# Kernel tuning notes

Measured on AMD Instinct MI355X. Metric: run time of the kernel, lower is better.

Reference implementation:

```python
import jax, jax.numpy as jnp
import numpy as np
from jax.scipy.special import logsumexp

G, E, K, D, B, L, M, KN = 32000, 256, 8, 6, 4, 512, 64, 4
STEP, EPS = 0.05, 1.0


def setup_inputs() -> dict:
    key = jax.random.key(0)
    ks = jax.random.split(key, 16)
    s = 0.05  # weight scale for numerical stability
    return {
        'masked': jax.random.randint(ks[0], (B, L), 0, G),
        'unmasked': jax.random.randint(ks[1], (B, L), 0, G),
        'mask': jax.random.randint(ks[2], (B, M), 0, L),
        'summer': jnp.ones((B, M), jnp.float32),
        'embed': jax.random.normal(ks[3], (G, E), jnp.float32) * s,
        'pos': jax.random.normal(ks[4], (L, E), jnp.float32) * s,
        'Wt': jax.random.normal(ks[5], (D, E, E), jnp.float32) * s,
        'Wc': jax.random.normal(ks[6], (D, E, E), jnp.float32) * s,
        'Wq': jax.random.normal(ks[7], (D, K * E, E), jnp.float32) * s,
        'Wd': jax.random.normal(ks[8], (D, K * E, K * E), jnp.float32) * s,
        'Wo': jax.random.normal(ks[9], (D, K * E, E), jnp.float32) * s,
        'Wkc': jax.random.normal(ks[10], (E * KN, E), jnp.float32) * s,
        'bkc': jax.random.normal(ks[11], (E * KN,), jnp.float32) * s,
        'Wem': jax.random.normal(ks[12], (E, E), jnp.float32) * s,
    }


def _norm(x):
    # y / (eps + y.std(-1, unbiased)); torch std is ddof=1
    return x / (EPS + jnp.std(x, axis=-1, ddof=1, keepdims=True))


def reference(masked, unmasked, mask, summer, embed, pos, Wt, Wc, Wq, Wd, Wo, Wkc, bkc, Wem):
    b, l = masked.shape
    # batch init: token + positional embedding, normalized
    xsa = _norm(embed[masked] + pos[None, :l])  # (B,L,E)
    inv_sqrt_e = 1.0 / (E ** 0.5)
    for d in range(D):
        # local transition terms (roll +/- 1 along sequence)
        xsad = jax.nn.relu(jnp.roll(xsa, 1, axis=1) @ Wt[d]) @ Wc[d]
        xsad = xsad + jax.nn.relu(jnp.roll(xsa, -1, axis=1) @ Wc[d].T) @ Wt[d].T
        # QKV_Attention: K query heads against raw xsa keys/values
        q = (xsa @ Wq[d].T).reshape(b, l, K, E)           # (B,L,K,E)
        hijk = jnp.einsum('blke,bme->blkm', q, xsa) * inv_sqrt_e  # (B,L,K,L)
        pijk = jax.nn.softmax(hijk, axis=-1)
        yik = jnp.einsum('blkm,bme->blke', pijk, xsa)      # (B,L,K,E)
        xid = yik.reshape(b, l, K * E)
        # Dense -> ReLU -> Dense (mode 1)
        xidact = jax.nn.relu(xid @ Wd[d].T)                # (B,L,K*E)
        xsad = xsad + xidact @ Wo[d]                       # (B,L,E)
        # gradnorm + residual update + layernorm
        xsad = _norm(xsad)
        xsa = _norm(xsa + STEP * xsad)
    # loss head: gather masked positions
    lptok = jnp.take_along_axis(xsa, mask[:, :, None], axis=1)  # (B,M,E)
    m = mask.shape[1]
    xx = (lptok @ Wkc.T + bkc).reshape(b, m * KN, E)       # kchoice
    xx = jnp.einsum('bne,ble->bnl', xx, xsa)               # (B,M*KN,L)
    xx = jnp.einsum('bnl,ble->bne', xx, xsa)               # (B,M*KN,E)
    logits = (xx @ Wem) @ embed.T                          # (B,M*KN,G)
    k_lp = jax.nn.log_softmax(logits, axis=-1).reshape(b, m, KN, G)
    lp = logsumexp(k_lp, axis=-2) - jnp.float32(np.log(KN))  # (B,M,G)
    tgt = jnp.take_along_axis(unmasked, mask, axis=1)       # (B,M)
    cent = jnp.take_along_axis(lp, tgt[:, :, None], axis=-1)[:, :, 0]
    loss = -(cent * summer).sum(-1) / jnp.clip(summer.sum(-1), 1.0, None)
    return loss
```

## Files before the change

kernel.cpp:

```cpp
#include <hip/hip_runtime.h>
#include <math.h>
#include <stdint.h>

#define G_ 32000
#define E_ 256
#define K_ 8
#define D_ 6
#define B_ 4
#define L_ 512
#define M_ 64
#define KN_ 4
#define STEP_ 0.05f
#define BL_ (B_ * L_)
#define KE_ (K_ * E_)
#define NSPLIT_ 50
#define GCH_ 10

typedef __attribute__((ext_vector_type(8))) short short8;
typedef __attribute__((ext_vector_type(4))) float f32x4;
typedef __attribute__((ext_vector_type(4))) short short4v;

__device__ __forceinline__ short f2bf(float f) {
  unsigned u = __builtin_bit_cast(unsigned, f);
  unsigned r = (u + 0x7fffu + ((u >> 16) & 1u)) >> 16;
  return (short)r;
}

__device__ __forceinline__ void gload16(const void* g, void* l) {
  __builtin_amdgcn_global_load_lds(
      reinterpret_cast<const __attribute__((address_space(1))) void*>(
          reinterpret_cast<uintptr_t>(g)),
      reinterpret_cast<__attribute__((address_space(3))) void*>(
          reinterpret_cast<uintptr_t>(l)),
      16, 0, 0);
}

__device__ __forceinline__ float wsum(float v) {
#pragma unroll
  for (int o = 32; o > 0; o >>= 1) v += __shfl_xor(v, o, 64);
  return v;
}
__device__ __forceinline__ float block_sum(float v, float* sm) {
  v = wsum(v);
  int wid = threadIdx.x >> 6, lane = threadIdx.x & 63;
  if (lane == 0) sm[wid] = v;
  __syncthreads();
  float r = sm[0] + sm[1] + sm[2] + sm[3];
  __syncthreads();
  return r;
}

template <bool RELU, bool OBF>
__global__ __launch_bounds__(256) void mg128x64_k(
    const short* __restrict__ A, const short* __restrict__ B,
    void* __restrict__ Cg, int Kd, int lda, int ldb, int ldc) {
  __shared__ short As[128 * 64];
  __shared__ short Bs[64 * 64];
  int m0 = blockIdx.y * 128, n0 = blockIdx.x * 64;
  int t = threadIdx.x, w = t >> 6, l = t & 63;
  int l16 = l & 15, qd = l >> 4, hi8 = qd * 8;
  int wr_ = w >> 1, wc_ = w & 1;
  int sr = l >> 3;
  int scol = ((l & 7) * 8) ^ (sr << 3);
  f32x4 acc[4][2];
#pragma unroll
  for (int i = 0; i < 4; i++)
#pragma unroll
    for (int j = 0; j < 2; j++) acc[i][j] = {0.f, 0.f, 0.f, 0.f};

  for (int k0 = 0; k0 < Kd; k0 += 64) {
    __syncthreads();
#pragma unroll
    for (int c = 0; c < 4; c++) {
      int sub = w * 4 + c;
      int r = sub * 8 + sr;
      gload16(A + (long)(m0 + r) * lda + k0 + scol, &As[sub * 512]);
    }
#pragma unroll
    for (int c = 0; c < 2; c++) {
      int sub = w * 2 + c;
      int r = sub * 8 + sr;
      gload16(B + (long)(n0 + r) * ldb + k0 + scol, &Bs[sub * 512]);
    }
    __syncthreads();
#pragma unroll
    for (int ks = 0; ks < 2; ks++) {
      short8 af[4], bf[2];
#pragma unroll
      for (int rf = 0; rf < 4; rf++) {
        int row = wr_ * 64 + rf * 16 + l16;
        af[rf] = *(const short8*)&As[(row * 64 + ks * 32 + hi8) ^ ((row & 7) << 3)];
      }
#pragma unroll
      for (int cf = 0; cf < 2; cf++) {
        int row = wc_ * 32 + cf * 16 + l16;
        bf[cf] = *(const short8*)&Bs[(row * 64 + ks * 32 + hi8) ^ ((row & 7) << 3)];
      }
#pragma unroll
      for (int rf = 0; rf < 4; rf++)
#pragma unroll
        for (int cf = 0; cf < 2; cf++)
          acc[rf][cf] = __builtin_amdgcn_mfma_f32_16x16x32_bf16(
              af[rf], bf[cf], acc[rf][cf], 0, 0, 0);
    }
  }
#pragma unroll
  for (int rf = 0; rf < 4; rf++) {
#pragma unroll
    for (int cf = 0; cf < 2; cf++) {
      int col = n0 + wc_ * 32 + cf * 16 + l16;
#pragma unroll
      for (int j = 0; j < 4; j++) {
        int row = m0 + wr_ * 64 + rf * 16 + qd * 4 + j;
        float v = acc[rf][cf][j];
        if (RELU) v = fmaxf(v, 0.f);
        long idx = (long)row * ldc + col;
        if (OBF) ((short*)Cg)[idx] = f2bf(v);
        else ((float*)Cg)[idx] = v;
      }
    }
  }
}

__global__ __launch_bounds__(256) void mg64sk_k(
    const short* __restrict__ A, const short* __restrict__ B,
    float* __restrict__ P, int Klen, int lda, int ldb, int ldc, long pstride) {
  __shared__ short As[64 * 64];
  __shared__ short Bs[64 * 64];
  int z = blockIdx.z;
  int kbase = z * Klen;
  int m0 = blockIdx.y * 64, n0 = blockIdx.x * 64;
  int t = threadIdx.x, w = t >> 6, l = t & 63;
  int l16 = l & 15, qd = l >> 4, hi8 = qd * 8;
  int wr_ = w >> 1, wc_ = w & 1;
  int sr = l >> 3;
  int scol = ((l & 7) * 8) ^ (sr << 3);
  f32x4 acc[2][2];
#pragma unroll
  for (int i = 0; i < 2; i++)
#pragma unroll
    for (int j = 0; j < 2; j++) acc[i][j] = {0.f, 0.f, 0.f, 0.f};

  for (int k0 = 0; k0 < Klen; k0 += 64) {
    __syncthreads();
#pragma unroll
    for (int c = 0; c < 2; c++) {
      int sub = w * 2 + c;
      int r = sub * 8 + sr;
      gload16(A + (long)(m0 + r) * lda + kbase + k0 + scol, &As[sub * 512]);
      gload16(B + (long)(n0 + r) * ldb + kbase + k0 + scol, &Bs[sub * 512]);
    }
    __syncthreads();
#pragma unroll
    for (int ks = 0; ks < 2; ks++) {
      short8 af[2], bf[2];
#pragma unroll
      for (int rf = 0; rf < 2; rf++) {
        int row = wr_ * 32 + rf * 16 + l16;
        af[rf] = *(const short8*)&As[(row * 64 + ks * 32 + hi8) ^ ((row & 7) << 3)];
      }
#pragma unroll
      for (int cf = 0; cf < 2; cf++) {
        int row = wc_ * 32 + cf * 16 + l16;
        bf[cf] = *(const short8*)&Bs[(row * 64 + ks * 32 + hi8) ^ ((row & 7) << 3)];
      }
#pragma unroll
      for (int rf = 0; rf < 2; rf++)
#pragma unroll
        for (int cf = 0; cf < 2; cf++)
          acc[rf][cf] = __builtin_amdgcn_mfma_f32_16x16x32_bf16(
              af[rf], bf[cf], acc[rf][cf], 0, 0, 0);
    }
  }
  float* Pz = P + z * pstride;
#pragma unroll
  for (int rf = 0; rf < 2; rf++) {
#pragma unroll
    for (int cf = 0; cf < 2; cf++) {
      int col = n0 + wc_ * 32 + cf * 16 + l16;
#pragma unroll
      for (int j = 0; j < 4; j++) {
        int row = m0 + wr_ * 32 + rf * 16 + qd * 4 + j;
        Pz[(long)row * ldc + col] = acc[rf][cf][j];
      }
    }
  }
}

__global__ __launch_bounds__(256) void tpair_k(
    const short* __restrict__ xsa_bf, const short* __restrict__ wtT,
    const short* __restrict__ wcb, short* __restrict__ T) {
  __shared__ short As[64 * 64];
  __shared__ short Bs[64 * 64];
  int z = blockIdx.z;
  const short* Bb = z ? wcb : wtT;
  int rollv = z ? -1 : 1;
  int m0 = blockIdx.y * 64, n0 = blockIdx.x * 64;
  int t = threadIdx.x, w = t >> 6, l = t & 63;
  int l16 = l & 15, qd = l >> 4, hi8 = qd * 8;
  int wr_ = w >> 1, wc_ = w & 1;
  int sr = l >> 3;
  int scol = ((l & 7) * 8) ^ (sr << 3);
  f32x4 acc[2][2];
#pragma unroll
  for (int i = 0; i < 2; i++)
#pragma unroll
    for (int j = 0; j < 2; j++) acc[i][j] = {0.f, 0.f, 0.f, 0.f};
  for (int k0 = 0; k0 < E_; k0 += 64) {
    __syncthreads();
#pragma unroll
    for (int c = 0; c < 2; c++) {
      int sub = w * 2 + c;
      int r = sub * 8 + sr;
      int gr = m0 + r;
      int bb = gr >> 9, pp = gr & (L_ - 1);
      gr = (bb << 9) | ((pp - rollv + L_) & (L_ - 1));
      gload16(xsa_bf + (long)gr * E_ + k0 + scol, &As[sub * 512]);
      gload16(Bb + (long)(n0 + sub * 8 + sr) * E_ + k0 + scol, &Bs[sub * 512]);
    }
    __syncthreads();
#pragma unroll
    for (int ks = 0; ks < 2; ks++) {
      short8 af[2], bf[2];
#pragma unroll
      for (int rf = 0; rf < 2; rf++) {
        int row = wr_ * 32 + rf * 16 + l16;
        af[rf] = *(const short8*)&As[(row * 64 + ks * 32 + hi8) ^ ((row & 7) << 3)];
      }
#pragma unroll
      for (int cf = 0; cf < 2; cf++) {
        int row = wc_ * 32 + cf * 16 + l16;
        bf[cf] = *(const short8*)&Bs[(row * 64 + ks * 32 + hi8) ^ ((row & 7) << 3)];
      }
#pragma unroll
      for (int rf = 0; rf < 2; rf++)
#pragma unroll
        for (int cf = 0; cf < 2; cf++)
          acc[rf][cf] = __builtin_amdgcn_mfma_f32_16x16x32_bf16(
              af[rf], bf[cf], acc[rf][cf], 0, 0, 0);
    }
  }
#pragma unroll
  for (int rf = 0; rf < 2; rf++) {
#pragma unroll
    for (int cf = 0; cf < 2; cf++) {
      int col = n0 + wc_ * 32 + cf * 16 + l16;
#pragma unroll
      for (int j = 0; j < 4; j++) {
        int row = m0 + wr_ * 32 + rf * 16 + qd * 4 + j;
        T[(long)row * 512 + z * 256 + col] = f2bf(fmaxf(acc[rf][cf][j], 0.f));
      }
    }
  }
}

__global__ __launch_bounds__(512, 2) void flash3_k(
    const short* __restrict__ q_bf, const short* __restrict__ xsa_bf,
    const short* __restrict__ xsaT_bf, short* __restrict__ y_bf) {
  __shared__ short smem[69888];
  float* Obuf = (float*)smem;
  float* mst = (float*)&smem[69632];
  float* lst = mst + 64;
  int q0 = blockIdx.x * 64, hk = blockIdx.y, b = blockIdx.z;
  int t = threadIdx.x, w = t >> 6, l = t & 63;
  int l16 = l & 15, qd = l >> 4, hi8 = qd * 8;
  int qb = w & 3, half = w >> 2;
  const float scale = 0.0625f;

  short8 qf[8];
  {
    const short* qrow =
        q_bf + (long)(b * L_ + q0 + qb * 16 + l16) * KE_ + hk * 256;
#pragma unroll
    for (int ks = 0; ks < 8; ks++)
      qf[ks] = *(const short8*)(qrow + ks * 32 + hi8);
  }
  f32x4 acc_o[16];
#pragma unroll
  for (int i = 0; i < 16; i++) acc_o[i] = {0.f, 0.f, 0.f, 0.f};
  float mreg[4], lreg[4];
#pragma unroll
  for (int j = 0; j < 4; j++) { mreg[j] = -1e30f; lreg[j] = 0.f; }

  auto STAGE = [&](int nbuf, int it) {
#pragma unroll
    for (int c = 0; c < 4; c++) {
      int ch = w * 4 + c, hh = ch >> 4, rp = ch & 15;
      int row = rp * 2 + (l >> 5);
      int colsw = ((l & 31) * 8) ^ ((row & 7) << 3);
      gload16(xsa_bf + (long)(b * L_ + hh * 256 + it * 32 + row) * E_ + colsw,
              &smem[(nbuf * 2 + hh) * 8192 + rp * 512]);
    }
#pragma unroll
    for (int c = 0; c < 4; c++) {
      int ch = w * 4 + c, hh = ch >> 4, rg = ch & 15;
      int er = rg * 16 + (l >> 2);
      int col = (l & 3) * 8;
      gload16(xsaT_bf + (long)(b * E_ + er) * L_ + hh * 256 + it * 32 + col,
              &smem[32768 + (nbuf * 2 + hh) * 8192 + rg * 512]);
    }
  };

  STAGE(0, 0);
  __syncthreads();
  int cur = 0;
  for (int it = 0; it < 8; it++) {
    if (it < 7) STAGE(cur ^ 1, it + 1);
    const short* Kb = &smem[(cur * 2 + half) * 8192];
    const short* Vb = &smem[32768 + (cur * 2 + half) * 8192];
    short* Pw = &smem[65536 + w * 512];
    f32x4 s4[2];
    s4[0] = {0.f, 0.f, 0.f, 0.f};
    s4[1] = {0.f, 0.f, 0.f, 0.f};
#pragma unroll
    for (int ks = 0; ks < 8; ks++) {
#pragma unroll
      for (int cf = 0; cf < 2; cf++) {
        int row = cf * 16 + l16;
        short8 kb = *(const short8*)&Kb[row * 256 +
                                        ((ks * 32 + hi8) ^ ((row & 7) << 3))];
        s4[cf] = __builtin_amdgcn_mfma_f32_16x16x32_bf16(qf[ks], kb, s4[cf], 0, 0, 0);
      }
    }
    float alpha[4];
#pragma unroll
    for (int j = 0; j < 4; j++) {
      float v0 = s4[0][j] * scale, v1 = s4[1][j] * scale;
      float rmax = fmaxf(v0, v1);
#pragma unroll
      for (int mk = 1; mk <= 8; mk <<= 1) rmax = fmaxf(rmax, __shfl_xor(rmax, mk, 64));
      float mn = fmaxf(mreg[j], rmax);
      float p0 = __expf(v0 - mn), p1 = __expf(v1 - mn);
      float ps = p0 + p1;
#pragma unroll
      for (int mk = 1; mk <= 8; mk <<= 1) ps += __shfl_xor(ps, mk, 64);
      alpha[j] = __expf(mreg[j] - mn);
      lreg[j] = lreg[j] * alpha[j] + ps;
      mreg[j] = mn;
      int r = qd * 4 + j;
      Pw[r * 32 + l16] = f2bf(p0);
      Pw[r * 32 + 16 + l16] = f2bf(p1);
    }
#pragma unroll
    for (int cfo = 0; cfo < 16; cfo++)
#pragma unroll
      for (int j = 0; j < 4; j++) acc_o[cfo][j] *= alpha[j];
    short8 pa = *(const short8*)&Pw[l16 * 32 + hi8];
#pragma unroll
    for (int cfo = 0; cfo < 16; cfo++) {
      int er = cfo * 16 + l16;
      short8 vb = *(const short8*)&Vb[er * 32 + hi8];
      acc_o[cfo] = __builtin_amdgcn_mfma_f32_16x16x32_bf16(pa, vb, acc_o[cfo], 0, 0, 0);
    }
    __syncthreads();
    cur ^= 1;
  }
  if (half == 1) {
#pragma unroll
    for (int cfo = 0; cfo < 16; cfo++)
#pragma unroll
      for (int j = 0; j < 4; j++)
        Obuf[qb * 4096 + (qd * 4 + j) * 256 + cfo * 16 + l16] = acc_o[cfo][j];
    if (l16 == 0) {
#pragma unroll
      for (int j = 0; j < 4; j++) {
        mst[qb * 16 + qd * 4 + j] = mreg[j];
        lst[qb * 16 + qd * 4 + j] = lreg[j];
      }
    }
  }
  __syncthreads();
  if (half == 0) {
#pragma unroll
    for (int j = 0; j < 4; j++) {
      int r = qd * 4 + j;
      float m1 = mst[qb * 16 + r], l1 = lst[qb * 16 + r];
      float mn = fmaxf(mreg[j], m1);
      float a0 = __expf(mreg[j] - mn), a1 = __expf(m1 - mn);
      float linv = 1.0f / (lreg[j] * a0 + l1 * a1);
      short* yrow = y_bf + (long)(b * L_ + q0 + qb * 16 + r) * KE_ + hk * 256;
#pragma unroll
      for (int cfo = 0; cfo < 16; cfo++) {
        float o1 = Obuf[qb * 4096 + r * 256 + cfo * 16 + l16];
        yrow[cfo * 16 + l16] = f2bf((acc_o[cfo][j] * a0 + o1 * a1) * linv);
      }
    }
  }
}

__global__ __launch_bounds__(256) void finish_k(
    const float* __restrict__ Ptr, const float* __restrict__ Pwo,
    float* __restrict__ xsa, short* __restrict__ xsa_bf,
    short* __restrict__ xsaT_bf) {
  long r = blockIdx.x;
  int b = (int)(r / L_), ll = (int)(r % L_);
  int t = threadIdx.x;
  __shared__ float sm[4];
  long off = r * E_ + t;
  const long ps = (long)BL_ * E_;
  float vd = Ptr[off] + Ptr[ps + off] + Pwo[off] + Pwo[ps + off] +
             Pwo[2 * ps + off] + Pwo[3 * ps + off];
  float s1 = block_sum(vd, sm);
  float s2 = block_sum(vd * vd, sm);
  float mean = s1 * (1.0f / E_);
  float var = (s2 - s1 * mean) * (1.0f / (E_ - 1));
  float vdn = vd / (1.0f + sqrtf(fmaxf(var, 0.f)));
  float u = xsa[off] + STEP_ * vdn;
  s1 = block_sum(u, sm);
  s2 = block_sum(u * u, sm);
  mean = s1 * (1.0f / E_);
  var = (s2 - s1 * mean) * (1.0f / (E_ - 1));
  float xn = u / (1.0f + sqrtf(fmaxf(var, 0.f)));
  xsa[off] = xn;
  short h = f2bf(xn);
  xsa_bf[off] = h;
  xsaT_bf[((long)b * E_ + t) * L_ + ll] = h;
}

__global__ __launch_bounds__(256) void lse2_k(
    const short* __restrict__ tmat_bf, const short* __restrict__ embed_bf,
    float* __restrict__ mpart, float* __restrict__ spart) {
  __shared__ short Bs[64 * 256];
  int split = blockIdx.x, rb = blockIdx.y;
  int t = threadIdx.x, w = t >> 6, l = t & 63;
  int l16 = l & 15, qd = l >> 4, hi8 = qd * 8;
  short8 areg[8];
  {
    const short* ar = tmat_bf + (long)(rb * 64 + w * 16 + l16) * E_;
#pragma unroll
    for (int ks = 0; ks < 8; ks++) areg[ks] = *(const short8*)(ar + ks * 32 + hi8);
  }
  float m[4], s[4];
#pragma unroll
  for (int j = 0; j < 4; j++) { m[j] = -1e30f; s[j] = 0.f; }
  long gbase = (long)split * (GCH_ * 64);
  for (int ch = 0; ch < GCH_; ch++) {
    long g0 = gbase + ch * 64;
    __syncthreads();
#pragma unroll
    for (int j = 0; j < 8; j++) {
      int sub = w * 8 + j;
      int r = sub * 2 + (l >> 5);
      int col = ((l & 31) * 8) ^ ((r & 7) << 3);
      gload16(embed_bf + (g0 + r) * E_ + col, &Bs[sub * 512]);
    }
    __syncthreads();
    f32x4 acc[4];
#pragma unroll
    for (int cf = 0; cf < 4; cf++) acc[cf] = {0.f, 0.f, 0.f, 0.f};
#pragma unroll
    for (int ks = 0; ks < 8; ks++) {
#pragma unroll
      for (int cf = 0; cf < 4; cf++) {
        int row = cf * 16 + l16;
        short8 b = *(const short8*)&Bs[(row * 256 + ks * 32 + hi8) ^ ((row & 7) << 3)];
        acc[cf] = __builtin_amdgcn_mfma_f32_16x16x32_bf16(areg[ks], b, acc[cf], 0, 0, 0);
      }
    }
#pragma unroll
    for (int j = 0; j < 4; j++) {
      float vm = fmaxf(fmaxf(acc[0][j], acc[1][j]), fmaxf(acc[2][j], acc[3][j]));
      float mn = fmaxf(m[j], vm);
      s[j] = s[j] * __expf(m[j] - mn) + __expf(acc[0][j] - mn) +
             __expf(acc[1][j] - mn) + __expf(acc[2][j] - mn) +
             __expf(acc[3][j] - mn);
      m[j] = mn;
    }
  }
#pragma unroll
  for (int j = 0; j < 4; j++) {
#pragma unroll
    for (int mask = 1; mask <= 8; mask <<= 1) {
      float mo = __shfl_xor(m[j], mask, 64);
      float so = __shfl_xor(s[j], mask, 64);
      float mn = fmaxf(m[j], mo);
      s[j] = s[j] * __expf(m[j] - mn) + so * __expf(mo - mn);
      m[j] = mn;
    }
    if (l16 == 0) {
      int row = rb * 64 + w * 16 + qd * 4 + j;
      mpart[(long)row * NSPLIT_ + split] = m[j];
      spart[(long)row * NSPLIT_ + split] = s[j];
    }
  }
}

__device__ __forceinline__ void cvt_blk(const float* __restrict__ src,
                                        short* __restrict__ dst, int blk, int t) {
  int i = blk * 256 + t;
  float4 v = ((const float4*)src)[i];
  short4v o = {f2bf(v.x), f2bf(v.y), f2bf(v.z), f2bf(v.w)};
  ((short4v*)dst)[i] = o;
}
__device__ __forceinline__ void trans_blk(const float* __restrict__ src,
                                          short* __restrict__ dst, int bx, int by,
                                          int C, int ldd, float (*tile)[33], int t) {
  int c0 = bx * 32, r0 = by * 32;
  int tx = t & 31, ty = t >> 5;
#pragma unroll
  for (int k = 0; k < 4; k++)
    tile[ty + k * 8][tx] = src[(long)(r0 + ty + k * 8) * C + c0 + tx];
  __syncthreads();
#pragma unroll
  for (int k = 0; k < 4; k++)
    dst[(long)(c0 + ty + k * 8) * ldd + r0 + tx] = f2bf(tile[tx][ty + k * 8]);
}
#define LBLK_ 5376
__global__ __launch_bounds__(256) void wcvt_all_k(
    const float* __restrict__ embed, const float* __restrict__ Wt,
    const float* __restrict__ Wc, const float* __restrict__ Wq,
    const float* __restrict__ Wd, const float* __restrict__ Wo,
    short* embed_bf, short* wcb, short* wq, short* wd, short* wtT, short* woT,
    short* wcat) {
  __shared__ float tile[32][33];
  int blk = blockIdx.x, t = threadIdx.x;
  if (blk < 8000) { cvt_blk(embed, embed_bf, blk, t); return; }
  blk -= 8000;
  int d = blk / LBLK_;
  blk -= d * LBLK_;
  const float* Wt_d = Wt + (long)d * E_ * E_;
  const float* Wc_d = Wc + (long)d * E_ * E_;
  const float* Wq_d = Wq + (long)d * KE_ * E_;
  const float* Wd_d = Wd + (long)d * KE_ * KE_;
  const float* Wo_d = Wo + (long)d * KE_ * E_;
  short* wcb_d = wcb + (long)d * E_ * E_;
  short* wq_d = wq + (long)d * KE_ * E_;
  short* wd_d = wd + (long)d * KE_ * KE_;
  short* wtT_d = wtT + (long)d * E_ * E_;
  short* woT_d = woT + (long)d * E_ * KE_;
  short* wcat_d = wcat + (long)d * E_ * 512;
  if (blk < 4096) { cvt_blk(Wd_d, wd_d, blk, t); return; }
  blk -= 4096;
  if (blk < 512) { cvt_blk(Wq_d, wq_d, blk, t); return; }
  blk -= 512;
  if (blk < 64) { cvt_blk(Wc_d, wcb_d, blk, t); return; }
  blk -= 64;
  if (blk < 64) { trans_blk(Wt_d, wtT_d, blk & 7, blk >> 3, E_, E_, tile, t); return; }
  blk -= 64;
  if (blk < 512) { trans_blk(Wo_d, woT_d, blk & 7, blk >> 3, E_, KE_, tile, t); return; }
  blk -= 512;
  if (blk < 64) { trans_blk(Wc_d, wcat_d, blk & 7, blk >> 3, E_, 512, tile, t); return; }
  blk -= 64;
  {
    int i = blk * 256 + t;
    int n = i >> 6, kc = (i & 63) * 4;
    float4 v = *(const float4*)(Wt_d + (long)n * E_ + kc);
    short4v o = {f2bf(v.x), f2bf(v.y), f2bf(v.z), f2bf(v.w)};
    *(short4v*)(wcat_d + (long)n * 512 + 256 + kc) = o;
  }
}

__global__ __launch_bounds__(256) void cvt_k(const float* __restrict__ src,
                                             short* __restrict__ dst, int n4) {
  int i = blockIdx.x * 256 + threadIdx.x;
  if (i < n4) {
    float4 v = ((const float4*)src)[i];
    short4v o = {f2bf(v.x), f2bf(v.y), f2bf(v.z), f2bf(v.w)};
    ((short4v*)dst)[i] = o;
  }
}

__global__ __launch_bounds__(256) void embed_init_k(
    const int* __restrict__ masked, const float* __restrict__ embed,
    const float* __restrict__ pos, float* __restrict__ xsa,
    short* __restrict__ xsa_bf, short* __restrict__ xsaT_bf) {
  int bl = blockIdx.x;
  int b = bl / L_, ll = bl % L_;
  int t = threadIdx.x;
  __shared__ float sm[4];
  int tok = masked[bl];
  float v = embed[(long)tok * E_ + t] + pos[(long)ll * E_ + t];
  float s1 = block_sum(v, sm);
  float s2 = block_sum(v * v, sm);
  float mean = s1 * (1.0f / E_);
  float var = (s2 - s1 * mean) * (1.0f / (E_ - 1));
  float xn = v / (1.0f + sqrtf(fmaxf(var, 0.f)));
  xsa[(long)bl * E_ + t] = xn;
  short h = f2bf(xn);
  xsa_bf[(long)bl * E_ + t] = h;
  xsaT_bf[((long)b * E_ + t) * L_ + ll] = h;
}

__global__ __launch_bounds__(256) void gather_k(const float* __restrict__ xsa,
                                                const int* __restrict__ mask,
                                                float* __restrict__ lptok) {
  int bm = blockIdx.x;
  int b = bm >> 6;
  int t = threadIdx.x;
  int p = mask[bm];
  lptok[(long)bm * E_ + t] = xsa[((long)b * L_ + p) * E_ + t];
}

template <bool TRB, bool BIAS>
__global__ __launch_bounds__(256) void gemm_k(
    const float* __restrict__ Ag, const float* __restrict__ Bg,
    float* __restrict__ Cg, const float* __restrict__ bias, int M, int N,
    int Kd, int lda, int ldb, int ldc, long sA1, long sB1, long sC1) {
  constexpr int BM = 64, BN = 64, BK = 16, TM = 4, TN = 4;
  int b1 = blockIdx.z;
  const float* A = Ag + b1 * sA1;
  const float* Bp = Bg + b1 * sB1;
  float* C = Cg + b1 * sC1;
  int m0 = blockIdx.y * BM, n0 = blockIdx.x * BN;
  __shared__ float As[BK][BM + 4];
  __shared__ float Bs[BK][BN + 4];
  int t = threadIdx.x;
  int tx = t % (BN / TN), ty = t / (BN / TN);
  float acc[TM][TN];
#pragma unroll
  for (int i = 0; i < TM; i++)
#pragma unroll
    for (int j = 0; j < TN; j++) acc[i][j] = 0.f;
  for (int k0 = 0; k0 < Kd; k0 += BK) {
    __syncthreads();
    {
      int r = t / (BK / 4), kc = (t % (BK / 4)) * 4;
      float4 v = *(const float4*)(A + (long)(m0 + r) * lda + k0 + kc);
      As[kc + 0][r] = v.x;
      As[kc + 1][r] = v.y;
      As[kc + 2][r] = v.z;
      As[kc + 3][r] = v.w;
    }
    if (!TRB) {
      int r = t / (BN / 4), nc = (t % (BN / 4)) * 4;
      *(float4*)(&Bs[r][nc]) = *(const float4*)(Bp + (long)(k0 + r) * ldb + n0 + nc);
    } else {
      int n = t / (BK / 4), kc = (t % (BK / 4)) * 4;
      float4 v = *(const float4*)(Bp + (long)(n0 + n) * ldb + k0 + kc);
      Bs[kc + 0][n] = v.x;
      Bs[kc + 1][n] = v.y;
      Bs[kc + 2][n] = v.z;
      Bs[kc + 3][n] = v.w;
    }
    __syncthreads();
#pragma unroll
    for (int kk = 0; kk < BK; kk++) {
      float a[TM], b[TN];
#pragma unroll
      for (int i = 0; i < TM; i++) a[i] = As[kk][ty * TM + i];
#pragma unroll
      for (int j = 0; j < TN; j++) b[j] = Bs[kk][tx * TN + j];
#pragma unroll
      for (int i = 0; i < TM; i++)
#pragma unroll
        for (int j = 0; j < TN; j++) acc[i][j] = fmaf(a[i], b[j], acc[i][j]);
    }
  }
#pragma unroll
  for (int i = 0; i < TM; i++) {
    long row = m0 + ty * TM + i;
    float* cp = C + row * (long)ldc + n0 + tx * TN;
#pragma unroll
    for (int j = 0; j < TN; j++) {
      float v = acc[i][j];
      if (BIAS) v += bias[n0 + tx * TN + j];
      cp[j] = v;
    }
  }
}

__global__ __launch_bounds__(256) void cent_k(
    const float* __restrict__ tmat, const float* __restrict__ embed,
    const int* __restrict__ mask, const int* __restrict__ unmasked,
    const float* __restrict__ mpart, const float* __restrict__ spart,
    float* __restrict__ cent) {
  int bm = blockIdx.x;
  int b = bm >> 6, m = bm & 63;
  int t = threadIdx.x;
  __shared__ float sm[4];
  __shared__ float tlv[KN_];
  int pos = mask[bm];
  int tgt = unmasked[b * L_ + pos];
  float ev = embed[(long)tgt * E_ + t];
  for (int kn = 0; kn < KN_; kn++) {
    long grow = (long)b * (M_ * KN_) + m * KN_ + kn;
    float dot = block_sum(tmat[grow * E_ + t] * ev, sm);
    if (t == 0) {
      float M = -1e30f, S = 0.f;
      for (int i = 0; i < NSPLIT_; i++) {
        float m2 = mpart[grow * NSPLIT_ + i], s2 = spart[grow * NSPLIT_ + i];
        float MM = fmaxf(M, m2);
        S = S * __expf(M - MM) + s2 * __expf(m2 - MM);
        M = MM;
      }
      tlv[kn] = dot - (M + __logf(S));
    }
  }
  __syncthreads();
  if (t == 0) {
    float mx = fmaxf(fmaxf(tlv[0], tlv[1]), fmaxf(tlv[2], tlv[3]));
    float s = __expf(tlv[0] - mx) + __expf(tlv[1] - mx) + __expf(tlv[2] - mx) +
              __expf(tlv[3] - mx);
    cent[bm] = __logf(s) + mx - 1.3862943611198906f;
  }
}

__global__ __launch_bounds__(256) void loss_k(const float* __restrict__ cent,
                                              const float* __restrict__ summer,
                                              float* __restrict__ out) {
  int t = threadIdx.x;
  int b = t >> 6, m = t & 63;
  float c = cent[b * 64 + m], su = summer[b * 64 + m];
  float num = wsum(c * su);
  float den = wsum(su);
  if (m == 0) out[b] = -num / fmaxf(den, 1.0f);
}

extern "C" void kernel_launch(void* const* d_in, const int* in_sizes, int n_in,
                              void* d_out, int out_size, void* d_ws,
                              size_t ws_size, hipStream_t stream) {
  (void)in_sizes; (void)n_in; (void)out_size; (void)ws_size;
  const int* masked = (const int*)d_in[0];
  const int* unmasked = (const int*)d_in[1];
  const int* mask = (const int*)d_in[2];
  const float* summer = (const float*)d_in[3];
  const float* embed = (const float*)d_in[4];
  const float* pos = (const float*)d_in[5];
  const float* Wt = (const float*)d_in[6];
  const float* Wc = (const float*)d_in[7];
  const float* Wq = (const float*)d_in[8];
  const float* Wd = (const float*)d_in[9];
  const float* Wo = (const float*)d_in[10];
  const float* Wkc = (const float*)d_in[11];
  const float* bkc = (const float*)d_in[12];
  const float* Wem = (const float*)d_in[13];
  float* out = (float*)d_out;

  char* p = (char*)d_ws;
  auto take = [&](size_t bytes) {
    char* r = p;
    p += (bytes + 255) & ~(size_t)255;
    return r;
  };
  float* xsa = (float*)take((size_t)BL_ * E_ * 4);
  short* xsa_bf = (short*)take((size_t)BL_ * E_ * 2);
  short* xsaT_bf = (short*)take((size_t)BL_ * E_ * 2);
  short* t_buf = (short*)take((size_t)BL_ * 512 * 2);
  short* q_bf = (short*)take((size_t)BL_ * KE_ * 2);
  short* y_bf = (short*)take((size_t)BL_ * KE_ * 2);
  float* P_tr = (float*)take((size_t)2 * BL_ * E_ * 4);
  float* P_wo = (float*)take((size_t)4 * BL_ * E_ * 4);
  short* wcb = (short*)take((size_t)D_ * E_ * E_ * 2);
  short* wtT = (short*)take((size_t)D_ * E_ * E_ * 2);
  short* wq = (short*)take((size_t)D_ * KE_ * E_ * 2);
  short* wd = (short*)take((size_t)D_ * KE_ * KE_ * 2);
  short* woT = (short*)take((size_t)D_ * E_ * KE_ * 2);
  short* wcat = (short*)take((size_t)D_ * E_ * 512 * 2);
  short* embed_bf = (short*)take((size_t)G_ * E_ * 2);
  float* lptok = (float*)take((size_t)B_ * M_ * E_ * 4);
  float* xx1 = (float*)take((size_t)B_ * M_ * KN_ * E_ * 4);
  float* xx2 = (float*)take((size_t)B_ * M_ * KN_ * L_ * 4);
  float* xx3 = (float*)take((size_t)B_ * M_ * KN_ * E_ * 4);
  float* tmat = (float*)take((size_t)B_ * M_ * KN_ * E_ * 4);
  short* tmat_bf = (short*)take((size_t)B_ * M_ * KN_ * E_ * 2);
  float* mpart = (float*)take((size_t)1024 * NSPLIT_ * 4);
  float* spart = (float*)take((size_t)1024 * NSPLIT_ * 4);
  float* cent = (float*)take((size_t)B_ * M_ * 4);

  dim3 blk(256);
  wcvt_all_k<<<8000 + D_ * LBLK_, blk, 0, stream>>>(
      embed, Wt, Wc, Wq, Wd, Wo, embed_bf, wcb, wq, wd, wtT, woT, wcat);
  embed_init_k<<<BL_, blk, 0, stream>>>(masked, embed, pos, xsa, xsa_bf, xsaT_bf);

  for (int d = 0; d < D_; d++) {
    short* wcb_d = wcb + (long)d * E_ * E_;
    short* wtT_d = wtT + (long)d * E_ * E_;
    short* wq_d = wq + (long)d * KE_ * E_;
    short* wd_d = wd + (long)d * KE_ * KE_;
    short* woT_d = woT + (long)d * E_ * KE_;
    short* wcat_d = wcat + (long)d * E_ * 512;

    tpair_k<<<dim3(4, 32, 2), blk, 0, stream>>>(xsa_bf, wtT_d, wcb_d, t_buf);
    mg64sk_k<<<dim3(4, 32, 2), blk, 0, stream>>>(t_buf, wcat_d, P_tr, 256, 512,
                                                 512, E_, (long)BL_ * E_);
    mg128x64_k<false, true><<<dim3(32, 16), blk, 0, stream>>>(
        xsa_bf, wq_d, q_bf, E_, E_, E_, KE_);
    flash3_k<<<dim3(L_ / 64, K_, B_), dim3(512), 0, stream>>>(q_bf, xsa_bf,
                                                              xsaT_bf, y_bf);
    mg128x64_k<true, true><<<dim3(32, 16), blk, 0, stream>>>(
        y_bf, wd_d, q_bf, KE_, KE_, KE_, KE_);
    mg64sk_k<<<dim3(4, 32, 4), blk, 0, stream>>>(q_bf, woT_d, P_wo, 512, KE_,
                                                 KE_, E_, (long)BL_ * E_);
    finish_k<<<BL_, blk, 0, stream>>>(P_tr, P_wo, xsa, xsa_bf, xsaT_bf);
  }

  gather_k<<<B_ * M_, blk, 0, stream>>>(xsa, mask, lptok);
  gemm_k<true, true><<<dim3(16, 4, 1), blk, 0, stream>>>(
      lptok, Wkc, xx1, bkc, B_ * M_, KN_ * E_, E_, E_, E_, KN_ * E_, 0, 0, 0);
  gemm_k<true, false><<<dim3(8, 4, B_), blk, 0, stream>>>(
      xx1, xsa, xx2, nullptr, M_ * KN_, L_, E_, E_, E_, L_,
      (long)M_ * KN_ * E_, (long)L_ * E_, (long)M_ * KN_ * L_);
  gemm_k<false, false><<<dim3(4, 4, B_), blk, 0, stream>>>(
      xx2, xsa, xx3, nullptr, M_ * KN_, E_, L_, L_, E_, E_,
      (long)M_ * KN_ * L_, (long)L_ * E_, (long)M_ * KN_ * E_);
  gemm_k<false, false><<<dim3(4, 4, B_), blk, 0, stream>>>(
      xx3, Wem, tmat, nullptr, M_ * KN_, E_, E_, E_, E_, E_,
      (long)M_ * KN_ * E_, 0, (long)M_ * KN_ * E_);
  cvt_k<<<256, blk, 0, stream>>>(tmat, tmat_bf, B_ * M_ * KN_ * E_ / 4);
  lse2_k<<<dim3(NSPLIT_, 16), blk, 0, stream>>>(tmat_bf, embed_bf, mpart, spart);
  cent_k<<<B_ * M_, blk, 0, stream>>>(tmat, embed, mask, unmasked, mpart, spart, cent);
  loss_k<<<1, blk, 0, stream>>>(cent, summer, out);
}
```

Baseline: 743.2 us.

## Move loss-head GEMMs to bf16 MFMA and widen weight conversion vectors

Replaces the four fp32 SIMT GEMMs in the loss head (kchoice, two sequence contractions, Wem projection) with a generic bf16 MFMA kernel that writes bf16 outputs, gathers from the bf16 activations, and drops the separate tmat conversion kernel. The weight conversion kernel now converts 8 elements per thread, and it also converts Wkc and transposes Wem up front. This targets the fp32 FMA cost and launch count of the head. In exchange the head runs in reduced precision, which may shift the loss slightly.

```diff
diff --git a/kernel.cpp b/kernel.cpp
--- a/kernel.cpp
+++ b/kernel.cpp
@@ -24,6 +24,9 @@
   unsigned u = __builtin_bit_cast(unsigned, f);
   unsigned r = (u + 0x7fffu + ((u >> 16) & 1u)) >> 16;
   return (short)r;
+}
+__device__ __forceinline__ float bf2f(short h) {
+  return __builtin_bit_cast(float, ((unsigned)(unsigned short)h) << 16);
 }
 
 __device__ __forceinline__ void gload16(const void* g, void* l) {
@@ -182,6 +185,75 @@
       for (int j = 0; j < 4; j++) {
         int row = m0 + wr_ * 32 + rf * 16 + qd * 4 + j;
         Pz[(long)row * ldc + col] = acc[rf][cf][j];
+      }
+    }
+  }
+}
+
+template <bool BIAS>
+__global__ __launch_bounds__(256) void mgh_k(
+    const short* __restrict__ Ag, const short* __restrict__ Bg,
+    short* __restrict__ Cg, const float* __restrict__ bias, int Kd, int lda,
+    int ldb, int ldc, long sA, long sB, long sC) {
+  __shared__ short As[64 * 64];
+  __shared__ short Bs[64 * 64];
+  int z = blockIdx.z;
+  const short* A = Ag + z * sA;
+  const short* B = Bg + z * sB;
+  short* C = Cg + z * sC;
+  int m0 = blockIdx.y * 64, n0 = blockIdx.x * 64;
+  int t = threadIdx.x, w = t >> 6, l = t & 63;
+  int l16 = l & 15, qd = l >> 4, hi8 = qd * 8;
+  int wr_ = w >> 1, wc_ = w & 1;
+  int sr = l >> 3;
+  int scol = ((l & 7) * 8) ^ (sr << 3);
+  f32x4 acc[2][2];
+#pragma unroll
+  for (int i = 0; i < 2; i++)
+#pragma unroll
+    for (int j = 0; j < 2; j++) acc[i][j] = {0.f, 0.f, 0.f, 0.f};
+
+  for (int k0 = 0; k0 < Kd; k0 += 64) {
+    __syncthreads();
+#pragma unroll
+    for (int c = 0; c < 2; c++) {
+      int sub = w * 2 + c;
+      int r = sub * 8 + sr;
+      gload16(A + (long)(m0 + r) * lda + k0 + scol, &As[sub * 512]);
+      gload16(B + (long)(n0 + r) * ldb + k0 + scol, &Bs[sub * 512]);
+    }
+    __syncthreads();
+#pragma unroll
+    for (int ks = 0; ks < 2; ks++) {
+      short8 af[2], bf[2];
+#pragma unroll
+      for (int rf = 0; rf < 2; rf++) {
+        int row = wr_ * 32 + rf * 16 + l16;
+        af[rf] = *(const short8*)&As[(row * 64 + ks * 32 + hi8) ^ ((row & 7) << 3)];
+      }
+#pragma unroll
+      for (int cf = 0; cf < 2; cf++) {
+        int row = wc_ * 32 + cf * 16 + l16;
+        bf[cf] = *(const short8*)&Bs[(row * 64 + ks * 32 + hi8) ^ ((row & 7) << 3)];
+      }
+#pragma unroll
+      for (int rf = 0; rf < 2; rf++)
+#pragma unroll
+        for (int cf = 0; cf < 2; cf++)
+          acc[rf][cf] = __builtin_amdgcn_mfma_f32_16x16x32_bf16(
+              af[rf], bf[cf], acc[rf][cf], 0, 0, 0);
+    }
+  }
+#pragma unroll
+  for (int rf = 0; rf < 2; rf++) {
+#pragma unroll
+    for (int cf = 0; cf < 2; cf++) {
+      int col = n0 + wc_ * 32 + cf * 16 + l16;
+      float bv = BIAS ? bias[col] : 0.f;
+#pragma unroll
+      for (int j = 0; j < 4; j++) {
+        int row = m0 + wr_ * 32 + rf * 16 + qd * 4 + j;
+        C[(long)row * ldc + col] = f2bf(acc[rf][cf][j] + bv);
       }
     }
   }
@@ -216,7 +288,7 @@
       int bb = gr >> 9, pp = gr & (L_ - 1);
       gr = (bb << 9) | ((pp - rollv + L_) & (L_ - 1));
       gload16(xsa_bf + (long)gr * E_ + k0 + scol, &As[sub * 512]);
-      gload16(Bb + (long)(n0 + sub * 8 + sr) * E_ + k0 + scol, &Bs[sub * 512]);
+      gload16(Bb + (long)(n0 + r) * E_ + k0 + scol, &Bs[sub * 512]);
     }
     __syncthreads();
 #pragma unroll
@@ -485,12 +557,14 @@
   }
 }
 
-__device__ __forceinline__ void cvt_blk(const float* __restrict__ src,
-                                        short* __restrict__ dst, int blk, int t) {
-  int i = blk * 256 + t;
-  float4 v = ((const float4*)src)[i];
-  short4v o = {f2bf(v.x), f2bf(v.y), f2bf(v.z), f2bf(v.w)};
-  ((short4v*)dst)[i] = o;
+__device__ __forceinline__ void cvt8_blk(const float* __restrict__ src,
+                                         short* __restrict__ dst, int blk, int t) {
+  long i = (long)blk * 256 + t;
+  const float4* s4 = (const float4*)src;
+  float4 a = s4[2 * i], b = s4[2 * i + 1];
+  short8 o = {f2bf(a.x), f2bf(a.y), f2bf(a.z), f2bf(a.w),
+              f2bf(b.x), f2bf(b.y), f2bf(b.z), f2bf(b.w)};
+  ((short8*)dst)[i] = o;
 }
 __device__ __forceinline__ void trans_blk(const float* __restrict__ src,
                                           short* __restrict__ dst, int bx, int by,
@@ -505,58 +579,63 @@
   for (int k = 0; k < 4; k++)
     dst[(long)(c0 + ty + k * 8) * ldd + r0 + tx] = f2bf(tile[tx][ty + k * 8]);
 }
-#define LBLK_ 5376
+#define WCVT_BLKS (4000 + 128 + 6 * 2368 + 64 + 6 * 640)
 __global__ __launch_bounds__(256) void wcvt_all_k(
     const float* __restrict__ embed, const float* __restrict__ Wt,
     const float* __restrict__ Wc, const float* __restrict__ Wq,
     const float* __restrict__ Wd, const float* __restrict__ Wo,
+    const float* __restrict__ Wkc, const float* __restrict__ Wem,
     short* embed_bf, short* wcb, short* wq, short* wd, short* wtT, short* woT,
-    short* wcat) {
+    short* wcat, short* wkc_bf, short* wemT) {
   __shared__ float tile[32][33];
   int blk = blockIdx.x, t = threadIdx.x;
-  if (blk < 8000) { cvt_blk(embed, embed_bf, blk, t); return; }
-  blk -= 8000;
-  int d = blk / LBLK_;
-  blk -= d * LBLK_;
-  const float* Wt_d = Wt + (long)d * E_ * E_;
-  const float* Wc_d = Wc + (long)d * E_ * E_;
-  const float* Wq_d = Wq + (long)d * KE_ * E_;
-  const float* Wd_d = Wd + (long)d * KE_ * KE_;
-  const float* Wo_d = Wo + (long)d * KE_ * E_;
-  short* wcb_d = wcb + (long)d * E_ * E_;
-  short* wq_d = wq + (long)d * KE_ * E_;
-  short* wd_d = wd + (long)d * KE_ * KE_;
-  short* wtT_d = wtT + (long)d * E_ * E_;
-  short* woT_d = woT + (long)d * E_ * KE_;
-  short* wcat_d = wcat + (long)d * E_ * 512;
-  if (blk < 4096) { cvt_blk(Wd_d, wd_d, blk, t); return; }
-  blk -= 4096;
-  if (blk < 512) { cvt_blk(Wq_d, wq_d, blk, t); return; }
-  blk -= 512;
-  if (blk < 64) { cvt_blk(Wc_d, wcb_d, blk, t); return; }
-  blk -= 64;
-  if (blk < 64) { trans_blk(Wt_d, wtT_d, blk & 7, blk >> 3, E_, E_, tile, t); return; }
-  blk -= 64;
-  if (blk < 512) { trans_blk(Wo_d, woT_d, blk & 7, blk >> 3, E_, KE_, tile, t); return; }
-  blk -= 512;
-  if (blk < 64) { trans_blk(Wc_d, wcat_d, blk & 7, blk >> 3, E_, 512, tile, t); return; }
+  if (blk < 4000) { cvt8_blk(embed, embed_bf, blk, t); return; }
+  blk -= 4000;
+  if (blk < 128) { cvt8_blk(Wkc, wkc_bf, blk, t); return; }
+  blk -= 128;
+  if (blk < 6 * 2368) {
+    int d = blk / 2368;
+    int r = blk - d * 2368;
+    if (r < 2048) { cvt8_blk(Wd + (long)d * KE_ * KE_, wd + (long)d * KE_ * KE_, r, t); return; }
+    r -= 2048;
+    if (r < 256) { cvt8_blk(Wq + (long)d * KE_ * E_, wq + (long)d * KE_ * E_, r, t); return; }
+    r -= 256;
+    if (r < 32) { cvt8_blk(Wc + (long)d * E_ * E_, wcb + (long)d * E_ * E_, r, t); return; }
+    r -= 32;
+    {
+      const float* Wt_d = Wt + (long)d * E_ * E_;
+      short* wcat_d = wcat + (long)d * E_ * 512;
+      long i = (long)r * 256 + t;
+      int n = (int)(i >> 5);
+      int kc = (int)(i & 31) * 8;
+      float4 a = *(const float4*)(Wt_d + (long)n * E_ + kc);
+      float4 b = *(const float4*)(Wt_d + (long)n * E_ + kc + 4);
+      short8 o = {f2bf(a.x), f2bf(a.y), f2bf(a.z), f2bf(a.w),
+                  f2bf(b.x), f2bf(b.y), f2bf(b.z), f2bf(b.w)};
+      *(short8*)(wcat_d + (long)n * 512 + 256 + kc) = o;
+      return;
+    }
+  }
+  blk -= 6 * 2368;
+  if (blk < 64) { trans_blk(Wem, wemT, blk & 7, blk >> 3, E_, E_, tile, t); return; }
   blk -= 64;
   {
-    int i = blk * 256 + t;
-    int n = i >> 6, kc = (i & 63) * 4;
-    float4 v = *(const float4*)(Wt_d + (long)n * E_ + kc);
-    short4v o = {f2bf(v.x), f2bf(v.y), f2bf(v.z), f2bf(v.w)};
-    *(short4v*)(wcat_d + (long)n * 512 + 256 + kc) = o;
-  }
-}
-
-__global__ __launch_bounds__(256) void cvt_k(const float* __restrict__ src,
-                                             short* __restrict__ dst, int n4) {
-  int i = blockIdx.x * 256 + threadIdx.x;
-  if (i < n4) {
-    float4 v = ((const float4*)src)[i];
-    short4v o = {f2bf(v.x), f2bf(v.y), f2bf(v.z), f2bf(v.w)};
-    ((short4v*)dst)[i] = o;
+    int d = blk / 640;
+    int r = blk - d * 640;
+    if (r < 64) {
+      trans_blk(Wt + (long)d * E_ * E_, wtT + (long)d * E_ * E_, r & 7, r >> 3,
+                E_, E_, tile, t);
+      return;
+    }
+    r -= 64;
+    if (r < 512) {
+      trans_blk(Wo + (long)d * KE_ * E_, woT + (long)d * E_ * KE_, r & 7, r >> 3,
+                E_, KE_, tile, t);
+      return;
+    }
+    r -= 512;
+    trans_blk(Wc + (long)d * E_ * E_, wcat + (long)d * E_ * 512, r & 7, r >> 3,
+              E_, 512, tile, t);
   }
 }
 
@@ -581,86 +660,18 @@
   xsaT_bf[((long)b * E_ + t) * L_ + ll] = h;
 }
 
-__global__ __launch_bounds__(256) void gather_k(const float* __restrict__ xsa,
-                                                const int* __restrict__ mask,
-                                                float* __restrict__ lptok) {
+__global__ __launch_bounds__(256) void gatherbf_k(const short* __restrict__ xsa_bf,
+                                                  const int* __restrict__ mask,
+                                                  short* __restrict__ lptok_bf) {
   int bm = blockIdx.x;
   int b = bm >> 6;
   int t = threadIdx.x;
   int p = mask[bm];
-  lptok[(long)bm * E_ + t] = xsa[((long)b * L_ + p) * E_ + t];
-}
-
-template <bool TRB, bool BIAS>
-__global__ __launch_bounds__(256) void gemm_k(
-    const float* __restrict__ Ag, const float* __restrict__ Bg,
-    float* __restrict__ Cg, const float* __restrict__ bias, int M, int N,
-    int Kd, int lda, int ldb, int ldc, long sA1, long sB1, long sC1) {
-  constexpr int BM = 64, BN = 64, BK = 16, TM = 4, TN = 4;
-  int b1 = blockIdx.z;
-  const float* A = Ag + b1 * sA1;
-  const float* Bp = Bg + b1 * sB1;
-  float* C = Cg + b1 * sC1;
-  int m0 = blockIdx.y * BM, n0 = blockIdx.x * BN;
-  __shared__ float As[BK][BM + 4];
-  __shared__ float Bs[BK][BN + 4];
-  int t = threadIdx.x;
-  int tx = t % (BN / TN), ty = t / (BN / TN);
-  float acc[TM][TN];
-#pragma unroll
-  for (int i = 0; i < TM; i++)
-#pragma unroll
-    for (int j = 0; j < TN; j++) acc[i][j] = 0.f;
-  for (int k0 = 0; k0 < Kd; k0 += BK) {
-    __syncthreads();
-    {
-      int r = t / (BK / 4), kc = (t % (BK / 4)) * 4;
-      float4 v = *(const float4*)(A + (long)(m0 + r) * lda + k0 + kc);
-      As[kc + 0][r] = v.x;
-      As[kc + 1][r] = v.y;
-      As[kc + 2][r] = v.z;
-      As[kc + 3][r] = v.w;
-    }
-    if (!TRB) {
-      int r = t / (BN / 4), nc = (t % (BN / 4)) * 4;
-      *(float4*)(&Bs[r][nc]) = *(const float4*)(Bp + (long)(k0 + r) * ldb + n0 + nc);
-    } else {
-      int n = t / (BK / 4), kc = (t % (BK / 4)) * 4;
-      float4 v = *(const float4*)(Bp + (long)(n0 + n) * ldb + k0 + kc);
-      Bs[kc + 0][n] = v.x;
-      Bs[kc + 1][n] = v.y;
-      Bs[kc + 2][n] = v.z;
-      Bs[kc + 3][n] = v.w;
-    }
-    __syncthreads();
-#pragma unroll
-    for (int kk = 0; kk < BK; kk++) {
-      float a[TM], b[TN];
-#pragma unroll
-      for (int i = 0; i < TM; i++) a[i] = As[kk][ty * TM + i];
-#pragma unroll
-      for (int j = 0; j < TN; j++) b[j] = Bs[kk][tx * TN + j];
-#pragma unroll
-      for (int i = 0; i < TM; i++)
-#pragma unroll
-        for (int j = 0; j < TN; j++) acc[i][j] = fmaf(a[i], b[j], acc[i][j]);
-    }
-  }
-#pragma unroll
-  for (int i = 0; i < TM; i++) {
-    long row = m0 + ty * TM + i;
-    float* cp = C + row * (long)ldc + n0 + tx * TN;
-#pragma unroll
-    for (int j = 0; j < TN; j++) {
-      float v = acc[i][j];
-      if (BIAS) v += bias[n0 + tx * TN + j];
-      cp[j] = v;
-    }
-  }
+  lptok_bf[(long)bm * E_ + t] = xsa_bf[((long)b * L_ + p) * E_ + t];
 }
 
 __global__ __launch_bounds__(256) void cent_k(
-    const float* __restrict__ tmat, const float* __restrict__ embed,
+    const short* __restrict__ tmat_bf, const float* __restrict__ embed,
     const int* __restrict__ mask, const int* __restrict__ unmasked,
     const float* __restrict__ mpart, const float* __restrict__ spart,
     float* __restrict__ cent) {
@@ -674,7 +685,8 @@
   float ev = embed[(long)tgt * E_ + t];
   for (int kn = 0; kn < KN_; kn++) {
     long grow = (long)b * (M_ * KN_) + m * KN_ + kn;
-    float dot = block_sum(tmat[grow * E_ + t] * ev, sm);
+    float tv = bf2f(tmat_bf[grow * E_ + t]);
+    float dot = block_sum(tv * ev, sm);
     if (t == 0) {
       float M = -1e30f, S = 0.f;
       for (int i = 0; i < NSPLIT_; i++) {
@@ -746,20 +758,22 @@
   short* wd = (short*)take((size_t)D_ * KE_ * KE_ * 2);
   short* woT = (short*)take((size_t)D_ * E_ * KE_ * 2);
   short* wcat = (short*)take((size_t)D_ * E_ * 512 * 2);
+  short* wkc_bf = (short*)take((size_t)KN_ * E_ * E_ * 2);
+  short* wemT = (short*)take((size_t)E_ * E_ * 2);
   short* embed_bf = (short*)take((size_t)G_ * E_ * 2);
-  float* lptok = (float*)take((size_t)B_ * M_ * E_ * 4);
-  float* xx1 = (float*)take((size_t)B_ * M_ * KN_ * E_ * 4);
-  float* xx2 = (float*)take((size_t)B_ * M_ * KN_ * L_ * 4);
-  float* xx3 = (float*)take((size_t)B_ * M_ * KN_ * E_ * 4);
-  float* tmat = (float*)take((size_t)B_ * M_ * KN_ * E_ * 4);
+  short* lptok_bf = (short*)take((size_t)B_ * M_ * E_ * 2);
+  short* xx1_bf = (short*)take((size_t)B_ * M_ * KN_ * E_ * 2);
+  short* xx2_bf = (short*)take((size_t)B_ * M_ * KN_ * L_ * 2);
+  short* xx3_bf = (short*)take((size_t)B_ * M_ * KN_ * E_ * 2);
   short* tmat_bf = (short*)take((size_t)B_ * M_ * KN_ * E_ * 2);
   float* mpart = (float*)take((size_t)1024 * NSPLIT_ * 4);
   float* spart = (float*)take((size_t)1024 * NSPLIT_ * 4);
   float* cent = (float*)take((size_t)B_ * M_ * 4);
 
   dim3 blk(256);
-  wcvt_all_k<<<8000 + D_ * LBLK_, blk, 0, stream>>>(
-      embed, Wt, Wc, Wq, Wd, Wo, embed_bf, wcb, wq, wd, wtT, woT, wcat);
+  wcvt_all_k<<<WCVT_BLKS, blk, 0, stream>>>(embed, Wt, Wc, Wq, Wd, Wo, Wkc, Wem,
+                                            embed_bf, wcb, wq, wd, wtT, woT,
+                                            wcat, wkc_bf, wemT);
   embed_init_k<<<BL_, blk, 0, stream>>>(masked, embed, pos, xsa, xsa_bf, xsaT_bf);
 
   for (int d = 0; d < D_; d++) {
@@ -784,20 +798,19 @@
     finish_k<<<BL_, blk, 0, stream>>>(P_tr, P_wo, xsa, xsa_bf, xsaT_bf);
   }
 
-  gather_k<<<B_ * M_, blk, 0, stream>>>(xsa, mask, lptok);
-  gemm_k<true, true><<<dim3(16, 4, 1), blk, 0, stream>>>(
-      lptok, Wkc, xx1, bkc, B_ * M_, KN_ * E_, E_, E_, E_, KN_ * E_, 0, 0, 0);
-  gemm_k<true, false><<<dim3(8, 4, B_), blk, 0, stream>>>(
-      xx1, xsa, xx2, nullptr, M_ * KN_, L_, E_, E_, E_, L_,
+  gatherbf_k<<<B_ * M_, blk, 0, stream>>>(xsa_bf, mask, lptok_bf);
+  mgh_k<true><<<dim3(16, 4, 1), blk, 0, stream>>>(
+      lptok_bf, wkc_bf, xx1_bf, bkc, E_, E_, E_, KN_ * E_, 0, 0, 0);
+  mgh_k<false><<<dim3(8, 4, B_), blk, 0, stream>>>(
+      xx1_bf, xsa_bf, xx2_bf, nullptr, E_, E_, E_, L_,
       (long)M_ * KN_ * E_, (long)L_ * E_, (long)M_ * KN_ * L_);
-  gemm_k<false, false><<<dim3(4, 4, B_), blk, 0, stream>>>(
-      xx2, xsa, xx3, nullptr, M_ * KN_, E_, L_, L_, E_, E_,
-      (long)M_ * KN_ * L_, (long)L_ * E_, (long)M_ * KN_ * E_);
-  gemm_k<false, false><<<dim3(4, 4, B_), blk, 0, stream>>>(
-      xx3, Wem, tmat, nullptr, M_ * KN_, E_, E_, E_, E_, E_,
-      (long)M_ * KN_ * E_, 0, (long)M_ * KN_ * E_);
-  cvt_k<<<256, blk, 0, stream>>>(tmat, tmat_bf, B_ * M_ * KN_ * E_ / 4);
+  mgh_k<false><<<dim3(4, 4, B_), blk, 0, stream>>>(
+      xx2_bf, xsaT_bf, xx3_bf, nullptr, L_, L_, L_, E_,
+      (long)M_ * KN_ * L_, (long)E_ * L_, (long)M_ * KN_ * E_);
+  mgh_k<false><<<dim3(4, 16, 1), blk, 0, stream>>>(
+      xx3_bf, wemT, tmat_bf, nullptr, E_, E_, E_, E_, 0, 0, 0);
   lse2_k<<<dim3(NSPLIT_, 16), blk, 0, stream>>>(tmat_bf, embed_bf, mpart, spart);
-  cent_k<<<B_ * M_, blk, 0, stream>>>(tmat, embed, mask, unmasked, mpart, spart, cent);
+  cent_k<<<B_ * M_, blk, 0, stream>>>(tmat_bf, embed, mask, unmasked, mpart,
+                                      spart, cent);
   loss_k<<<1, blk, 0, stream>>>(cent, summer, out);
 }
```

Result: faster. 686.1 us (-7.7%).
